# Optimization experiments

Hardware: AMD Instinct MI355X
Metric: run time of the kernel (lower is better)

## Reference

```python
import jax, jax.numpy as jnp
import numpy as np

B, T, D = 64, 4096, 256
UNITS = 256  # must equal D due to the module's build() wiring


def setup_inputs() -> dict:
    key = jax.random.key(0)
    k1, k2, k3 = jax.random.split(key, 3)
    inputs = jax.random.normal(k1, (B, T, D), dtype=jnp.float32)
    # Glorot-uniform-ish init for Dense kernels, zeros for biases (Keras defaults)
    lim_w = np.sqrt(6.0 / (D + UNITS)).astype(np.float32)
    W_w = jax.random.uniform(k2, (D, UNITS), jnp.float32, -lim_w, lim_w)
    W_b = jnp.zeros((UNITS,), jnp.float32)
    lim_v = np.sqrt(6.0 / (UNITS + 1)).astype(np.float32)
    V_w = jax.random.uniform(k3, (UNITS, 1), jnp.float32, -lim_v, lim_v)
    V_b = jnp.zeros((1,), jnp.float32)
    return {"inputs": inputs, "W_w": W_w, "W_b": W_b, "V_w": V_w, "V_b": V_b}


def reference(inputs, W_w, W_b, V_w, V_b):
    # score: [B, T, UNITS]
    score = jnp.tanh(jnp.einsum('btd,du->btu', inputs, W_w) + W_b)
    # logits: [B, T, 1]; softmax over time axis (axis=1)
    logits = jnp.einsum('btu,uo->bto', score, V_w) + V_b
    attn = jax.nn.softmax(logits, axis=1)  # [B, T, 1]
    # weighted sum over time -> [B, D]
    context = jnp.sum(attn * inputs, axis=1)
    return context
```

## Files before the change

### kernel.cpp

```cpp
#include <hip/hip_runtime.h>
#include <hip/hip_bf16.h>
#include <math.h>

#define BB 64
#define TT 4096
#define DD 256
#define UU 256
#define CHUNKS 8
#define TCHUNK 512
#define MT 64
#define NTILES 8
#define LDA 264

typedef __attribute__((ext_vector_type(8))) short bf16x8;
typedef __attribute__((ext_vector_type(4))) float f32x4;

static __device__ __forceinline__ short f2bf(float f){
  unsigned u = __float_as_uint(f);
  u = (u + 0x7fffu + ((u >> 16) & 1u)) >> 16;
  return (short)u;
}

__global__ void wconv_kernel(const float* __restrict__ W, short* __restrict__ Wt){
  int u = blockIdx.x;
  int d = threadIdx.x;
  Wt[u*DD + d] = f2bf(W[d*UU + u]);
}

__global__ __launch_bounds__(256)
void attn_main_kernel(const float* __restrict__ X, const short* __restrict__ Wt,
                      const float* __restrict__ Wb, const float* __restrict__ Vw,
                      float* __restrict__ m_part, float* __restrict__ l_part,
                      float* __restrict__ ctx_part)
{
  __shared__ short a_tile[MT*LDA];
  __shared__ float s_logits[MT];
  __shared__ float s_p[MT];
  __shared__ float s_m, s_l, s_alpha;

  const int tid  = threadIdx.x;
  const int lane = tid & 63;
  const int wv   = tid >> 6;
  const int b    = blockIdx.x >> 3;
  const int cchunk = blockIdx.x & 7;
  const int lo   = lane & 15;
  const int quad = lane >> 4;
  const int u_base = wv*64 + lo;

  if (tid == 0){ s_m = -INFINITY; s_l = 0.f; }

  float wb_r[4], v_r[4];
  #pragma unroll
  for (int nf=0; nf<4; ++nf){
    wb_r[nf] = Wb[u_base + nf*16];
    v_r[nf]  = Vw[u_base + nf*16];
  }

  float ctx = 0.f;
  const size_t x_chunk = ((size_t)b*TT + (size_t)cchunk*TCHUNK) * DD;

  for (int tile=0; tile<NTILES; ++tile){
    const int t0 = tile*MT;

    if (tid < MT) s_logits[tid] = 0.f;
    #pragma unroll
    for (int p8=0; p8<8; ++p8){
      int e   = p8*256 + tid;
      int row = e >> 5;
      int col = (e & 31) * 8;
      const float4* src = reinterpret_cast<const float4*>(
          X + x_chunk + (size_t)(t0+row)*DD + col);
      float4 x0 = src[0];
      float4 x1 = src[1];
      bf16x8 v;
      v[0]=f2bf(x0.x); v[1]=f2bf(x0.y); v[2]=f2bf(x0.z); v[3]=f2bf(x0.w);
      v[4]=f2bf(x1.x); v[5]=f2bf(x1.y); v[6]=f2bf(x1.z); v[7]=f2bf(x1.w);
      *reinterpret_cast<bf16x8*>(&a_tile[row*LDA + col]) = v;
    }
    __syncthreads();

    f32x4 acc[4][4];
    #pragma unroll
    for (int mf=0; mf<4; ++mf)
      #pragma unroll
      for (int nf=0; nf<4; ++nf)
        acc[mf][nf] = (f32x4){0.f,0.f,0.f,0.f};

    #pragma unroll
    for (int kt=0; kt<8; ++kt){
      const int k0 = kt*32 + quad*8;
      bf16x8 af[4];
      #pragma unroll
      for (int mf=0; mf<4; ++mf)
        af[mf] = *reinterpret_cast<const bf16x8*>(&a_tile[(mf*16 + lo)*LDA + k0]);
      #pragma unroll
      for (int nf=0; nf<4; ++nf){
        bf16x8 bfv = *reinterpret_cast<const bf16x8*>(&Wt[(size_t)(u_base + nf*16)*DD + k0]);
        #pragma unroll
        for (int mf=0; mf<4; ++mf)
          acc[mf][nf] = __builtin_amdgcn_mfma_f32_16x16x32_bf16(af[mf], bfv, acc[mf][nf], 0, 0, 0);
      }
    }

    #pragma unroll
    for (int mf=0; mf<4; ++mf){
      #pragma unroll
      for (int r=0; r<4; ++r){
        float part = 0.f;
        #pragma unroll
        for (int nf=0; nf<4; ++nf){
          float s  = acc[mf][nf][r] + wb_r[nf];
          float e2 = __expf(2.f*s);
          float th = 1.f - 2.f/(e2 + 1.f);
          part = fmaf(th, v_r[nf], part);
        }
        part += __shfl_xor(part, 1);
        part += __shfl_xor(part, 2);
        part += __shfl_xor(part, 4);
        part += __shfl_xor(part, 8);
        if (lo == 0) atomicAdd(&s_logits[mf*16 + quad*4 + r], part);
      }
    }
    __syncthreads();

    if (tid < MT){
      float lt = s_logits[tid];
      float mx = lt;
      #pragma unroll
      for (int o=32; o; o>>=1) mx = fmaxf(mx, __shfl_xor(mx, o));
      float m_old = s_m;
      float m_new = fmaxf(m_old, mx);
      float p = __expf(lt - m_new);
      s_p[tid] = p;
      float sum = p;
      #pragma unroll
      for (int o=32; o; o>>=1) sum += __shfl_xor(sum, o);
      if (tid == 0){
        float alpha = __expf(m_old - m_new);
        s_alpha = alpha;
        s_l = s_l * alpha + sum;
        s_m = m_new;
      }
    }
    __syncthreads();

    float alpha = s_alpha;
    ctx *= alpha;
    const float* xcol = X + x_chunk + (size_t)t0*DD + tid;
    #pragma unroll
    for (int t2=0; t2<MT; ++t2)
      ctx = fmaf(s_p[t2], xcol[(size_t)t2*DD], ctx);
  }

  __syncthreads();
  const int pidx = b*CHUNKS + cchunk;
  if (tid == 0){ m_part[pidx] = s_m; l_part[pidx] = s_l; }
  ctx_part[(size_t)pidx*DD + tid] = ctx;
}

__global__ void merge_kernel(const float* __restrict__ m_part, const float* __restrict__ l_part,
                             const float* __restrict__ ctx_part, float* __restrict__ out)
{
  int b = blockIdx.x;
  int d = threadIdx.x;
  float mg = -INFINITY;
  #pragma unroll
  for (int c=0; c<CHUNKS; ++c) mg = fmaxf(mg, m_part[b*CHUNKS+c]);
  float lg = 0.f, s = 0.f;
  #pragma unroll
  for (int c=0; c<CHUNKS; ++c){
    float w = __expf(m_part[b*CHUNKS+c] - mg);
    lg += l_part[b*CHUNKS+c] * w;
    s  += ctx_part[(size_t)(b*CHUNKS+c)*DD + d] * w;
  }
  out[b*DD + d] = s / lg;
}

extern "C" void kernel_launch(void* const* d_in, const int* in_sizes, int n_in,
                              void* d_out, int out_size, void* d_ws, size_t ws_size,
                              hipStream_t stream)
{
  const float* X  = (const float*)d_in[0];
  const float* Ww = (const float*)d_in[1];
  const float* Wb = (const float*)d_in[2];
  const float* Vw = (const float*)d_in[3];
  float* out = (float*)d_out;

  short* Wt     = (short*)d_ws;
  float* m_part = (float*)((char*)d_ws + (size_t)UU*DD*sizeof(short));
  float* l_part = m_part + BB*CHUNKS;
  float* ctx_part = l_part + BB*CHUNKS;

  wconv_kernel<<<UU, DD, 0, stream>>>(Ww, Wt);
  attn_main_kernel<<<BB*CHUNKS, 256, 0, stream>>>(X, Wt, Wb, Vw, m_part, l_part, ctx_part);
  merge_kernel<<<BB, DD, 0, stream>>>(m_part, l_part, ctx_part, out);
}
```

Baseline: 445.3 us.

## Split time into more chunks and reuse LDS bf16 tile for the context sum

Quadruples the number of time chunks per batch, from 512 to 2048 blocks, to raise occupancy across the CUs. Each wave now writes its logit partials to its own shared slot instead of using shared-memory atomics. Every wave then computes the online-softmax state redundantly in registers, which removes one barrier and the shared softmax scalars. The weighted context sum reads the bf16-converted X tile already in LDS instead of re-reading fp32 X from global memory, halving global traffic. In exchange the context is computed from bf16-rounded inputs, and the merge kernel has more partials to combine.

```diff
diff --git a/kernel.cpp b/kernel.cpp
--- a/kernel.cpp
+++ b/kernel.cpp
@@ -6,10 +6,10 @@
 #define TT 4096
 #define DD 256
 #define UU 256
-#define CHUNKS 8
-#define TCHUNK 512
+#define CHUNKS 32
+#define TCHUNK 128
 #define MT 64
-#define NTILES 8
+#define NTILES 2
 #define LDA 264
 
 typedef __attribute__((ext_vector_type(8))) short bf16x8;
@@ -34,20 +34,17 @@
                       float* __restrict__ ctx_part)
 {
   __shared__ short a_tile[MT*LDA];
-  __shared__ float s_logits[MT];
-  __shared__ float s_p[MT];
-  __shared__ float s_m, s_l, s_alpha;
+  __shared__ float s_part[4][MT];
+  __shared__ float s_pw[4][MT];
 
   const int tid  = threadIdx.x;
   const int lane = tid & 63;
   const int wv   = tid >> 6;
-  const int b    = blockIdx.x >> 3;
-  const int cchunk = blockIdx.x & 7;
+  const int b      = blockIdx.x >> 5;
+  const int cchunk = blockIdx.x & 31;
   const int lo   = lane & 15;
   const int quad = lane >> 4;
   const int u_base = wv*64 + lo;
-
-  if (tid == 0){ s_m = -INFINITY; s_l = 0.f; }
 
   float wb_r[4], v_r[4];
   #pragma unroll
@@ -56,13 +53,15 @@
     v_r[nf]  = Vw[u_base + nf*16];
   }
 
-  float ctx = 0.f;
+  float m_run = -INFINITY;
+  float l_run = 0.f;
+  float ctx   = 0.f;
   const size_t x_chunk = ((size_t)b*TT + (size_t)cchunk*TCHUNK) * DD;
 
   for (int tile=0; tile<NTILES; ++tile){
+    __syncthreads();
     const int t0 = tile*MT;
 
-    if (tid < MT) s_logits[tid] = 0.f;
     #pragma unroll
     for (int p8=0; p8<8; ++p8){
       int e   = p8*256 + tid;
@@ -118,43 +117,37 @@
         part += __shfl_xor(part, 2);
         part += __shfl_xor(part, 4);
         part += __shfl_xor(part, 8);
-        if (lo == 0) atomicAdd(&s_logits[mf*16 + quad*4 + r], part);
+        if (lo == 0) s_part[wv][mf*16 + quad*4 + r] = part;
       }
     }
     __syncthreads();
 
-    if (tid < MT){
-      float lt = s_logits[tid];
-      float mx = lt;
-      #pragma unroll
-      for (int o=32; o; o>>=1) mx = fmaxf(mx, __shfl_xor(mx, o));
-      float m_old = s_m;
-      float m_new = fmaxf(m_old, mx);
-      float p = __expf(lt - m_new);
-      s_p[tid] = p;
-      float sum = p;
-      #pragma unroll
-      for (int o=32; o; o>>=1) sum += __shfl_xor(sum, o);
-      if (tid == 0){
-        float alpha = __expf(m_old - m_new);
-        s_alpha = alpha;
-        s_l = s_l * alpha + sum;
-        s_m = m_new;
-      }
+    float lt = s_part[0][lane] + s_part[1][lane] + s_part[2][lane] + s_part[3][lane];
+    float mx = lt;
+    #pragma unroll
+    for (int o=32; o; o>>=1) mx = fmaxf(mx, __shfl_xor(mx, o));
+    float m_new = fmaxf(m_run, mx);
+    float p = __expf(lt - m_new);
+    float sum = p;
+    #pragma unroll
+    for (int o=32; o; o>>=1) sum += __shfl_xor(sum, o);
+    float alpha = __expf(m_run - m_new);
+    l_run = l_run * alpha + sum;
+    m_run = m_new;
+    s_pw[wv][lane] = p;
+
+    ctx *= alpha;
+    #pragma unroll
+    for (int t2=0; t2<MT; ++t2){
+      float pt = s_pw[wv][t2];
+      unsigned xb = (unsigned short)a_tile[t2*LDA + tid];
+      float xv = __uint_as_float(xb << 16);
+      ctx = fmaf(pt, xv, ctx);
     }
-    __syncthreads();
-
-    float alpha = s_alpha;
-    ctx *= alpha;
-    const float* xcol = X + x_chunk + (size_t)t0*DD + tid;
-    #pragma unroll
-    for (int t2=0; t2<MT; ++t2)
-      ctx = fmaf(s_p[t2], xcol[(size_t)t2*DD], ctx);
   }
 
-  __syncthreads();
-  const int pidx = b*CHUNKS + cchunk;
-  if (tid == 0){ m_part[pidx] = s_m; l_part[pidx] = s_l; }
+  const int pidx = blockIdx.x;
+  if (tid == 0){ m_part[pidx] = m_run; l_part[pidx] = l_run; }
   ctx_part[(size_t)pidx*DD + tid] = ctx;
 }
 
@@ -186,9 +179,9 @@
   const float* Vw = (const float*)d_in[3];
   float* out = (float*)d_out;
 
-  short* Wt     = (short*)d_ws;
-  float* m_part = (float*)((char*)d_ws + (size_t)UU*DD*sizeof(short));
-  float* l_part = m_part + BB*CHUNKS;
+  short* Wt       = (short*)d_ws;
+  float* m_part   = (float*)((char*)d_ws + (size_t)UU*DD*sizeof(short));
+  float* l_part   = m_part + BB*CHUNKS;
   float* ctx_part = l_part + BB*CHUNKS;
 
   wconv_kernel<<<UU, DD, 0, stream>>>(Ww, Wt);
```

Result: slower. 510.3 us (+14.6%).
